# Kernel tuning notes

Hardware: AMD Instinct MI355X
Metric: run time of the kernel (lower is better)

Reference implementation:

```python
import jax, jax.numpy as jnp
import numpy as np

N_NODES = 50000
N_EDGES = 800000
HIDDEN = 64


def _init_linear(key, fan_in, fan_out):
    kw, kb = jax.random.split(key)
    lim = 1.0 / np.sqrt(fan_in)
    W = jax.random.uniform(kw, (fan_in, fan_out), jnp.float32, -lim, lim)
    b = jax.random.uniform(kb, (fan_out,), jnp.float32, -lim, lim)
    return W, b


def setup_inputs() -> dict:
    key = jax.random.key(0)
    ks = jax.random.split(key, 10)
    feat = jax.random.normal(ks[0], (N_NODES, HIDDEN), jnp.float32)
    x = jax.random.normal(ks[1], (N_NODES, 3), jnp.float32)
    src = jax.random.randint(ks[2], (N_EDGES,), 0, N_NODES, jnp.int32)
    dst = jax.random.randint(ks[3], (N_EDGES,), 0, N_NODES, jnp.int32)
    # message MLP: (2H+1) -> H -> H, relu after both layers (last_activation=mid)
    W1, b1 = _init_linear(ks[4], 2 * HIDDEN + 1, HIDDEN)
    W2, b2 = _init_linear(ks[5], HIDDEN, HIDDEN)
    # soft edge gate: H -> 1
    we, be = _init_linear(ks[6], HIDDEN, 1)
    # update MLP: H -> H -> H, relu mid, no last activation
    U1, c1 = _init_linear(ks[7], HIDDEN, HIDDEN)
    U2, c2 = _init_linear(ks[8], HIDDEN, HIDDEN)
    return dict(feat=feat, x=x, src=src, dst=dst,
                W1=W1, b1=b1, W2=W2, b2=b2, we=we, be=be,
                U1=U1, c1=c1, U2=U2, c2=c2)


def reference(feat, x, src, dst, W1, b1, W2, b2, we, be, U1, c1, U2, c2):
    # per-edge squared distance between endpoint coordinates: [E, 1]
    sqd = jnp.sum((x[src] - x[dst]) ** 2, axis=-1, keepdims=True)
    # message input: [E, 2H+1]
    msg_in = jnp.concatenate([feat[src], feat[dst], sqd], axis=-1)
    # 2-layer message MLP with relu mid and last activation
    m = jax.nn.relu(jax.nn.relu(msg_in @ W1 + b1) @ W2 + b2)
    # sigmoid soft-edge gate: [E, 1]
    gate = jax.nn.sigmoid(m @ we + be)
    # scatter-sum gated messages to destination nodes: [N, H]
    m_sum = jax.ops.segment_sum(m * gate, dst, num_segments=N_NODES)
    # node update MLP on (m_sum + feat), residual add
    h = m_sum + feat
    h_new = jax.nn.relu(h @ U1 + c1) @ U2 + c2
    return h_new + feat
```

## Files before the change

kernel.cpp:

```cpp
#include <hip/hip_runtime.h>
#include <hip/hip_bf16.h>
#include <stdint.h>

#define N_NODES 50000
#define N_EDGES 800000
#define HDIM 64
#define SCAN_N (N_NODES + 1)

#define MSUM_OFF   0
#define EP_OFF     12800000
#define DEG_OFF    (EP_OFF + 12800000)
#define OFFS_OFF   (DEG_OFF + 204800)
#define POS_OFF    (OFFS_OFF + 204800)
#define FB_OFF     (POS_OFF + 204800)
#define W1T_OFF    (FB_OFF + (size_t)N_NODES * HDIM * 2)
#define W2T_OFF    (W1T_OFF + 16384)
#define U1T_OFF    (W2T_OFF + 8192)
#define U2T_OFF    (U1T_OFF + 8192)
#define CST_OFF    (U2T_OFF + 8192)
#define WS_NEED    (CST_OFF + 4096)

#define CVT_BLOCKS   1563
#define PREPW_BLOCKS 82
#define MZ_BLOCKS    3125
#define HIST_BLOCKS  1024

typedef __attribute__((ext_vector_type(8))) short short8;
typedef __attribute__((ext_vector_type(4))) float floatx4;

__device__ __forceinline__ float bf2f(unsigned short u) {
    union { unsigned int i; float f; } v; v.i = ((unsigned int)u) << 16; return v.f;
}
__device__ __forceinline__ unsigned short f2bf(float f) {
    __hip_bfloat16 h = __float2bfloat16(f);
    return *reinterpret_cast<unsigned short*>(&h);
}

__device__ __forceinline__ int detect_is_bf16(const unsigned short* p) {
    int cnt = 0;
    #pragma unroll
    for (int i = 0; i < 64; ++i) {
        unsigned short b = p[i];
        int e = (b >> 7) & 0xFF;
        cnt += ((e >= 97 && e <= 157) || (b & 0x7FFF) == 0) ? 1 : 0;
    }
    return cnt >= 56;
}

__device__ __forceinline__ float getf(const void* p, unsigned int i, int isb) {
    return isb ? bf2f(((const unsigned short*)p)[i]) : ((const float*)p)[i];
}

__device__ __forceinline__ short8 get8bf(const void* p, unsigned int i, int isb) {
    if (isb) {
        return *reinterpret_cast<const short8*>((const short*)p + i);
    } else {
        const float4 f0 = *reinterpret_cast<const float4*>((const float*)p + i);
        const float4 f1 = *reinterpret_cast<const float4*>((const float*)p + i + 4);
        short8 a;
        a[0] = (short)f2bf(f0.x); a[1] = (short)f2bf(f0.y);
        a[2] = (short)f2bf(f0.z); a[3] = (short)f2bf(f0.w);
        a[4] = (short)f2bf(f1.x); a[5] = (short)f2bf(f1.y);
        a[6] = (short)f2bf(f1.z); a[7] = (short)f2bf(f1.w);
        return a;
    }
}

#define COMPILER_FENCE() asm volatile("" ::: "memory")
#define WAIT_LDS() __builtin_amdgcn_s_waitcnt(0xC07F)

__global__ __launch_bounds__(256) void prep_kernel(
    const void* __restrict__ feat, unsigned short* __restrict__ fb,
    const void* __restrict__ W1, const void* __restrict__ W2,
    const void* __restrict__ U1, const void* __restrict__ U2,
    const void* __restrict__ b1, const void* __restrict__ b2,
    const void* __restrict__ we, const void* __restrict__ be,
    unsigned short* __restrict__ w1t, unsigned short* __restrict__ w2t,
    unsigned short* __restrict__ u1t, unsigned short* __restrict__ u2t,
    float* __restrict__ cst,
    const int* __restrict__ dst, int* __restrict__ deg,
    uint4* __restrict__ msumz)
{
    const int b = blockIdx.x;
    if (b < CVT_BLOCKS) {
        const int isb = detect_is_bf16((const unsigned short*)feat);
        int i = (b * 256 + threadIdx.x) * 8;
        if (i >= N_NODES * HDIM) return;
        if (isb) {
            *reinterpret_cast<uint4*>(fb + i) =
                *reinterpret_cast<const uint4*>((const unsigned short*)feat + i);
        } else {
            float4 f0 = *reinterpret_cast<const float4*>((const float*)feat + i);
            float4 f1 = *reinterpret_cast<const float4*>((const float*)feat + i + 4);
            ushort4 a = {f2bf(f0.x), f2bf(f0.y), f2bf(f0.z), f2bf(f0.w)};
            ushort4 c = {f2bf(f1.x), f2bf(f1.y), f2bf(f1.z), f2bf(f1.w)};
            *reinterpret_cast<ushort4*>(fb + i)     = a;
            *reinterpret_cast<ushort4*>(fb + i + 4) = c;
        }
    } else if (b < CVT_BLOCKS + PREPW_BLOCKS) {
        const int isb = detect_is_bf16((const unsigned short*)feat);
        int idx = (b - CVT_BLOCKS) * 256 + threadIdx.x;
        if (idx < 8192) {
            int n = idx >> 7, k = idx & 127;
            w1t[idx] = f2bf(getf(W1, k * 64 + n, isb));
        } else if (idx < 12288) {
            int i = idx - 8192, n = i >> 6, k = i & 63;
            w2t[i] = f2bf(getf(W2, k * 64 + n, isb));
        } else if (idx < 16384) {
            int i = idx - 12288, n = i >> 6, k = i & 63;
            u1t[i] = f2bf(getf(U1, k * 64 + n, isb));
        } else if (idx < 20480) {
            int i = idx - 16384, n = i >> 6, k = i & 63;
            u2t[i] = f2bf(getf(U2, k * 64 + n, isb));
        } else if (idx < 20737) {
            int i = idx - 20480;
            float v;
            if (i < 64)       v = getf(b1, i, isb);
            else if (i < 128) v = getf(W1, 128 * 64 + (i - 64), isb);
            else if (i < 192) v = getf(b2, i - 128, isb);
            else if (i < 256) v = getf(we, i - 192, isb);
            else              v = getf(be, 0, isb);
            cst[i] = v;
        }
    } else if (b < CVT_BLOCKS + PREPW_BLOCKS + MZ_BLOCKS) {
        int i = (b - CVT_BLOCKS - PREPW_BLOCKS) * 256 + threadIdx.x;
        if (i < N_NODES * HDIM / 4)
            msumz[i] = (uint4){0u, 0u, 0u, 0u};
    } else {
        int e0 = (b - CVT_BLOCKS - PREPW_BLOCKS - MZ_BLOCKS) * 256 + threadIdx.x;
        for (int e = e0; e < N_EDGES; e += HIST_BLOCKS * 256)
            atomicAdd(&deg[dst[e]], 1);
    }
}

__global__ __launch_bounds__(1024) void scan_onepass_kernel(
    const int* __restrict__ deg, int* __restrict__ offs, int* __restrict__ pos)
{
    __shared__ int wsum[16];
    const int tid  = threadIdx.x;
    const int wid  = tid >> 6;
    const int lane = tid & 63;
    int run = 0;
    for (int seg = 0; seg < 49; ++seg) {
        int g = seg * 1024 + tid;
        int v = (g < SCAN_N) ? deg[g] : 0;
        int x = v;
        #pragma unroll
        for (int off = 1; off < 64; off <<= 1) {
            int t = __shfl_up(x, off);
            if (lane >= off) x += t;
        }
        if (lane == 63) wsum[wid] = x;
        __syncthreads();
        if (wid == 0) {
            int w = (lane < 16) ? wsum[lane] : 0;
            #pragma unroll
            for (int off = 1; off < 16; off <<= 1) {
                int t = __shfl_up(w, off);
                if (lane >= off) w += t;
            }
            if (lane < 16) wsum[lane] = w;
        }
        __syncthreads();
        int wexcl = (wid == 0) ? 0 : wsum[wid - 1];
        int tot   = wsum[15];
        int excl  = run + wexcl + (x - v);
        if (g < SCAN_N) { offs[g] = excl; pos[g] = excl; }
        run += tot;
        __syncthreads();
    }
}

__global__ __launch_bounds__(256) void permute_kernel(
    const void* __restrict__ feat, const void* __restrict__ xpos,
    const int* __restrict__ src, const int* __restrict__ dst,
    int* __restrict__ pos, uint4* __restrict__ epack)
{
    const int isb = detect_is_bf16((const unsigned short*)feat);
    int e = blockIdx.x * 256 + threadIdx.x;
    if (e < N_EDGES) {
        int s = src[e], d = dst[e];
        int slot = atomicAdd(&pos[d], 1);
        float dx = getf(xpos, s * 3 + 0, isb) - getf(xpos, d * 3 + 0, isb);
        float dy = getf(xpos, s * 3 + 1, isb) - getf(xpos, d * 3 + 1, isb);
        float dz = getf(xpos, s * 3 + 2, isb) - getf(xpos, d * 3 + 2, isb);
        float sqd = dx * dx + dy * dy + dz * dz;
        uint4 p;
        p.x = (unsigned int)s;
        p.y = (unsigned int)d;
        p.z = __float_as_uint(sqd);
        p.w = 0u;
        epack[slot] = p;
    }
}

template <bool CSR>
__global__ __launch_bounds__(512, 4) void edge_kernel(
    const unsigned short* __restrict__ fbf,
    const unsigned short* __restrict__ w1t, const unsigned short* __restrict__ w2t,
    const float* __restrict__ cst,
    const void* __restrict__ feat, const void* __restrict__ xpos,
    const int* __restrict__ src, const int* __restrict__ dst,
    const uint4* __restrict__ epack,
    const void* __restrict__ W1, const void* __restrict__ b1,
    const void* __restrict__ W2, const void* __restrict__ b2,
    const void* __restrict__ we, const void* __restrict__ be,
    float* __restrict__ msum, unsigned int msum_cap)
{
    __shared__ __align__(16) short sW1[16][64][8];
    __shared__ __align__(16) short sW2[8][64][8];
    __shared__ __align__(16) short sA2[2][8][16][72];

    const int tid  = threadIdx.x;
    const int wave = tid >> 6;
    const int lane = tid & 63;
    const int l15  = lane & 15;
    const int quad = lane >> 4;
    const int rowb = quad * 4;

    float b1r[4], w1lr[4], b2r[4], wer[4];
    float ber;
    short8 bw1[4][4];
    short8 bw2[2][4];

    if constexpr (CSR) {
        for (int i = tid; i < 16 * 64; i += 512) {
            int f = i >> 6, l = i & 63;
            int n = (f & 3) * 16 + (l & 15);
            int k0 = (f >> 2) * 32 + (l >> 4) * 8;
            *reinterpret_cast<short8*>(&sW1[f][l][0]) =
                *reinterpret_cast<const short8*>(w1t + n * 128 + k0);
        }
        for (int i = tid; i < 8 * 64; i += 512) {
            int f = i >> 6, l = i & 63;
            int n = (f & 3) * 16 + (l & 15);
            int k0 = (f >> 2) * 32 + (l >> 4) * 8;
            *reinterpret_cast<short8*>(&sW2[f][l][0]) =
                *reinterpret_cast<const short8*>(w2t + n * 64 + k0);
        }
        #pragma unroll
        for (int nt = 0; nt < 4; ++nt) {
            int n = nt * 16 + l15;
            b1r[nt]  = cst[n];
            w1lr[nt] = cst[64 + n];
            b2r[nt]  = cst[128 + n];
            wer[nt]  = cst[192 + n];
        }
        ber = cst[256];
        __syncthreads();

        const int nbiter = N_EDGES / 256;
        for (int it = blockIdx.x; it < nbiter; it += gridDim.x) {
            const int ebase = it * 256 + wave * 16;

            int sidx = 0, didx = 0;
            float sqd = 0.f;
            if (lane < 32) {
                int e = ebase + l15 + ((lane >> 4) << 7);
                uint4 p = epack[e];
                sidx = (int)p.x;
                didx = (int)p.y;
                sqd  = __uint_as_float(p.z);
            }
            const int snA = __shfl(sidx, l15);
            const int dnA = __shfl(didx, l15);
            const int snB = __shfl(sidx, l15 + 16);
            const int dnB = __shfl(didx, l15 + 16);

            short8 caA[4], caB[4];
            #pragma unroll
            for (int c = 0; c < 4; ++c) {
                const int nA = (c < 2) ? snA : dnA;
                const int nB = (c < 2) ? snB : dnB;
                caA[c] = *reinterpret_cast<const short8*>(
                    (const short*)fbf + (unsigned int)nA * 64u + (c & 1) * 32 + quad * 8);
                caB[c] = *reinterpret_cast<const short8*>(
                    (const short*)fbf + (unsigned int)nB * 64u + (c & 1) * 32 + quad * 8);
            }

            floatx4 accA[4], accB[4];
            #pragma unroll
            for (int nt = 0; nt < 4; ++nt) {
                accA[nt] = (floatx4){0.f, 0.f, 0.f, 0.f};
                accB[nt] = (floatx4){0.f, 0.f, 0.f, 0.f};
            }
            #pragma unroll
            for (int c = 0; c < 4; ++c) {
                #pragma unroll
                for (int nt = 0; nt < 4; ++nt) {
                    short8 wb = *reinterpret_cast<const short8*>(&sW1[c * 4 + nt][lane][0]);
                    accA[nt] = __builtin_amdgcn_mfma_f32_16x16x32_bf16(caA[c], wb, accA[nt], 0, 0, 0);
                    accB[nt] = __builtin_amdgcn_mfma_f32_16x16x32_bf16(caB[c], wb, accB[nt], 0, 0, 0);
                }
            }

            float sqA[4], sqB[4];
            #pragma unroll
            for (int r = 0; r < 4; ++r) {
                sqA[r] = __shfl(sqd, rowb + r);
                sqB[r] = __shfl(sqd, 16 + rowb + r);
            }
            #pragma unroll
            for (int nt = 0; nt < 4; ++nt)
                #pragma unroll
                for (int r = 0; r < 4; ++r) {
                    float vA = fmaxf(accA[nt][r] + b1r[nt] + sqA[r] * w1lr[nt], 0.f);
                    float vB = fmaxf(accB[nt][r] + b1r[nt] + sqB[r] * w1lr[nt], 0.f);
                    sA2[0][wave][rowb + r][nt * 16 + l15] = (short)f2bf(vA);
                    sA2[1][wave][rowb + r][nt * 16 + l15] = (short)f2bf(vB);
                }
            COMPILER_FENCE();
            WAIT_LDS();

            floatx4 acc2A[4], acc2B[4];
            #pragma unroll
            for (int nt = 0; nt < 4; ++nt) {
                acc2A[nt] = (floatx4){0.f, 0.f, 0.f, 0.f};
                acc2B[nt] = (floatx4){0.f, 0.f, 0.f, 0.f};
            }
            #pragma unroll
            for (int c = 0; c < 2; ++c) {
                short8 aA = *reinterpret_cast<const short8*>(&sA2[0][wave][l15][c * 32 + quad * 8]);
                short8 aB = *reinterpret_cast<const short8*>(&sA2[1][wave][l15][c * 32 + quad * 8]);
                #pragma unroll
                for (int nt = 0; nt < 4; ++nt) {
                    short8 wb = *reinterpret_cast<const short8*>(&sW2[c * 4 + nt][lane][0]);
                    acc2A[nt] = __builtin_amdgcn_mfma_f32_16x16x32_bf16(aA, wb, acc2A[nt], 0, 0, 0);
                    acc2B[nt] = __builtin_amdgcn_mfma_f32_16x16x32_bf16(aB, wb, acc2B[nt], 0, 0, 0);
                }
            }
            COMPILER_FENCE();

            float mvA[4][4], mvB[4][4];
            float pA[4] = {0.f, 0.f, 0.f, 0.f};
            float pB[4] = {0.f, 0.f, 0.f, 0.f};
            #pragma unroll
            for (int nt = 0; nt < 4; ++nt)
                #pragma unroll
                for (int r = 0; r < 4; ++r) {
                    float vA = fmaxf(acc2A[nt][r] + b2r[nt], 0.f);
                    float vB = fmaxf(acc2B[nt][r] + b2r[nt], 0.f);
                    mvA[nt][r] = vA;
                    mvB[nt][r] = vB;
                    pA[r] += vA * wer[nt];
                    pB[r] += vB * wer[nt];
                }
            #pragma unroll
            for (int off = 1; off < 16; off <<= 1)
                #pragma unroll
                for (int r = 0; r < 4; ++r) {
                    pA[r] += __shfl_xor(pA[r], off);
                    pB[r] += __shfl_xor(pB[r], off);
                }
            float gA[4], gB[4];
            #pragma unroll
            for (int r = 0; r < 4; ++r) {
                gA[r] = 1.f / (1.f + __expf(-(pA[r] + ber)));
                gB[r] = 1.f / (1.f + __expf(-(pB[r] + ber)));
            }

            int grp = (lane >> 4) & 1;
            int nd = __shfl(didx, grp * 16 + ((l15 + 1) & 15));
            int flag = (lane < 32) && ((l15 == 15) || (nd != didx));
            unsigned long long bal = __ballot(flag);
            unsigned int mA = (unsigned int)(bal & 0xFFFFull);
            unsigned int mB = (unsigned int)((bal >> 16) & 0xFFFFull);

            int lo = 0;
            while (mA) {
                int hi = __ffs(mA) - 1;
                float s0 = 0.f, s1 = 0.f, s2 = 0.f, s3 = 0.f;
                #pragma unroll
                for (int r = 0; r < 4; ++r) {
                    int gr = rowb + r;
                    float g = (gr >= lo && gr <= hi) ? gA[r] : 0.f;
                    s0 += g * mvA[0][r];
                    s1 += g * mvA[1][r];
                    s2 += g * mvA[2][r];
                    s3 += g * mvA[3][r];
                }
                s0 += __shfl_xor(s0, 16); s0 += __shfl_xor(s0, 32);
                s1 += __shfl_xor(s1, 16); s1 += __shfl_xor(s1, 32);
                s2 += __shfl_xor(s2, 16); s2 += __shfl_xor(s2, 32);
                s3 += __shfl_xor(s3, 16); s3 += __shfl_xor(s3, 32);
                int d = __shfl(didx, hi);
                float v = (quad == 0) ? s0 : (quad == 1) ? s1 : (quad == 2) ? s2 : s3;
                unsafeAtomicAdd(&msum[(unsigned int)d * 64u + (unsigned int)quad * 16u + l15], v);
                lo = hi + 1;
                mA &= mA - 1;
            }
            lo = 0;
            while (mB) {
                int hi = __ffs(mB) - 1;
                float s0 = 0.f, s1 = 0.f, s2 = 0.f, s3 = 0.f;
                #pragma unroll
                for (int r = 0; r < 4; ++r) {
                    int gr = rowb + r;
                    float g = (gr >= lo && gr <= hi) ? gB[r] : 0.f;
                    s0 += g * mvB[0][r];
                    s1 += g * mvB[1][r];
                    s2 += g * mvB[2][r];
                    s3 += g * mvB[3][r];
                }
                s0 += __shfl_xor(s0, 16); s0 += __shfl_xor(s0, 32);
                s1 += __shfl_xor(s1, 16); s1 += __shfl_xor(s1, 32);
                s2 += __shfl_xor(s2, 16); s2 += __shfl_xor(s2, 32);
                s3 += __shfl_xor(s3, 16); s3 += __shfl_xor(s3, 32);
                int d = __shfl(didx, 16 + hi);
                float v = (quad == 0) ? s0 : (quad == 1) ? s1 : (quad == 2) ? s2 : s3;
                unsafeAtomicAdd(&msum[(unsigned int)d * 64u + (unsigned int)quad * 16u + l15], v);
                lo = hi + 1;
                mB &= mB - 1;
            }
        }
    } else {
        const int isb = detect_is_bf16((const unsigned short*)feat);
        #pragma unroll
        for (int c = 0; c < 4; ++c)
            #pragma unroll
            for (int nt = 0; nt < 4; ++nt) {
                short8 b;
                #pragma unroll
                for (int j = 0; j < 8; ++j)
                    b[j] = (short)f2bf(getf(W1, (c * 32 + quad * 8 + j) * 64 + nt * 16 + l15, isb));
                bw1[c][nt] = b;
            }
        #pragma unroll
        for (int c = 0; c < 2; ++c)
            #pragma unroll
            for (int nt = 0; nt < 4; ++nt) {
                short8 b;
                #pragma unroll
                for (int j = 0; j < 8; ++j)
                    b[j] = (short)f2bf(getf(W2, (c * 32 + quad * 8 + j) * 64 + nt * 16 + l15, isb));
                bw2[c][nt] = b;
            }
        #pragma unroll
        for (int nt = 0; nt < 4; ++nt) {
            int n = nt * 16 + l15;
            b1r[nt]  = getf(b1, n, isb);
            w1lr[nt] = getf(W1, 128 * 64 + n, isb);
            b2r[nt]  = getf(b2, n, isb);
            wer[nt]  = getf(we, n, isb);
        }
        ber = getf(be, 0, isb);

        const int ntiles = N_EDGES / 128;
        for (int t = blockIdx.x; t < ntiles; t += gridDim.x) {
            const int ebase = t * 128 + wave * 16;
            int sidx = 0, didx = 0;
            float sqd = 0.f;
            if (lane < 16) {
                int e = ebase + lane;
                sidx = src[e];
                didx = dst[e];
                float dx = getf(xpos, sidx * 3 + 0, isb) - getf(xpos, didx * 3 + 0, isb);
                float dy = getf(xpos, sidx * 3 + 1, isb) - getf(xpos, didx * 3 + 1, isb);
                float dz = getf(xpos, sidx * 3 + 2, isb) - getf(xpos, didx * 3 + 2, isb);
                sqd = dx * dx + dy * dy + dz * dz;
            }
            const int sn     = __shfl(sidx, l15);
            const int dn_row = __shfl(didx, l15);

            floatx4 acc[4];
            #pragma unroll
            for (int nt = 0; nt < 4; ++nt) acc[nt] = (floatx4){0.f, 0.f, 0.f, 0.f};
            #pragma unroll
            for (int c = 0; c < 4; ++c) {
                const int node = (c < 2) ? sn : dn_row;
                const unsigned int aoff = (unsigned int)node * 64u + (c & 1) * 32 + quad * 8;
                short8 a = get8bf(feat, aoff, isb);
                #pragma unroll
                for (int nt = 0; nt < 4; ++nt)
                    acc[nt] = __builtin_amdgcn_mfma_f32_16x16x32_bf16(a, bw1[c][nt], acc[nt], 0, 0, 0);
            }

            float sq[4];
            #pragma unroll
            for (int r = 0; r < 4; ++r) sq[r] = __shfl(sqd, rowb + r);
            #pragma unroll
            for (int nt = 0; nt < 4; ++nt)
                #pragma unroll
                for (int r = 0; r < 4; ++r) {
                    float v = fmaxf(acc[nt][r] + b1r[nt] + sq[r] * w1lr[nt], 0.f);
                    sA2[0][wave][rowb + r][nt * 16 + l15] = (short)f2bf(v);
                }
            COMPILER_FENCE();
            WAIT_LDS();

            floatx4 acc2[4];
            #pragma unroll
            for (int nt = 0; nt < 4; ++nt) acc2[nt] = (floatx4){0.f, 0.f, 0.f, 0.f};
            #pragma unroll
            for (int c = 0; c < 2; ++c) {
                short8 a = *reinterpret_cast<const short8*>(&sA2[0][wave][l15][c * 32 + quad * 8]);
                #pragma unroll
                for (int nt = 0; nt < 4; ++nt)
                    acc2[nt] = __builtin_amdgcn_mfma_f32_16x16x32_bf16(a, bw2[c][nt], acc2[nt], 0, 0, 0);
            }
            COMPILER_FENCE();

            float mval[4][4];
            float part[4] = {0.f, 0.f, 0.f, 0.f};
            #pragma unroll
            for (int nt = 0; nt < 4; ++nt)
                #pragma unroll
                for (int r = 0; r < 4; ++r) {
                    float v = fmaxf(acc2[nt][r] + b2r[nt], 0.f);
                    mval[nt][r] = v;
                    part[r] += v * wer[nt];
                }
            #pragma unroll
            for (int off = 1; off < 16; off <<= 1)
                #pragma unroll
                for (int r = 0; r < 4; ++r) part[r] += __shfl_xor(part[r], off);
            float gate[4];
            #pragma unroll
            for (int r = 0; r < 4; ++r)
                gate[r] = 1.f / (1.f + __expf(-(part[r] + ber)));

            #pragma unroll
            for (int r = 0; r < 4; ++r) {
                int dn = __shfl(didx, rowb + r);
                unsigned int base = (unsigned int)dn * 64u;
                if (base + 64u <= msum_cap) {
                    #pragma unroll
                    for (int nt = 0; nt < 4; ++nt)
                        unsafeAtomicAdd(&msum[base + nt * 16 + l15], mval[nt][r] * gate[r]);
                }
            }
        }
    }
}

__global__ __launch_bounds__(256, 2) void node_kernel(
    const float* __restrict__ msum,
    const unsigned short* __restrict__ u1t, const unsigned short* __restrict__ u2t,
    const void* __restrict__ feat,
    const void* __restrict__ U1, const void* __restrict__ c1v,
    const void* __restrict__ U2, const void* __restrict__ c2v,
    void* __restrict__ out)
{
    __shared__ __align__(16) short sT[4][16][72];
    __shared__ __align__(16) float sF[4][16][68];

    const int isb  = detect_is_bf16((const unsigned short*)feat);
    const int tid  = threadIdx.x;
    const int wave = tid >> 6;
    const int lane = tid & 63;
    const int l15  = lane & 15;
    const int quad = lane >> 4;

    short8 u1f[2][4], u2f[2][4];
    if (u1t) {
        #pragma unroll
        for (int nt = 0; nt < 4; ++nt) {
            const int n = nt * 16 + l15;
            #pragma unroll
            for (int c = 0; c < 2; ++c) {
                u1f[c][nt] = *reinterpret_cast<const short8*>(u1t + n * 64 + c * 32 + quad * 8);
                u2f[c][nt] = *reinterpret_cast<const short8*>(u2t + n * 64 + c * 32 + quad * 8);
            }
        }
    } else {
        #pragma unroll
        for (int c = 0; c < 2; ++c)
            #pragma unroll
            for (int nt = 0; nt < 4; ++nt) {
                short8 a, b;
                #pragma unroll
                for (int j = 0; j < 8; ++j) {
                    int k = c * 32 + quad * 8 + j, n = nt * 16 + l15;
                    a[j] = (short)f2bf(getf(U1, k * 64 + n, isb));
                    b[j] = (short)f2bf(getf(U2, k * 64 + n, isb));
                }
                u1f[c][nt] = a; u2f[c][nt] = b;
            }
    }
    float c1r[4], c2r[4];
    #pragma unroll
    for (int nt = 0; nt < 4; ++nt) {
        c1r[nt] = getf(c1v, nt * 16 + l15, isb);
        c2r[nt] = getf(c2v, nt * 16 + l15, isb);
    }
    const int rowb = quad * 4;

    const int ntile = (N_NODES + 15) / 16;
    const int t = blockIdx.x * 4 + wave;
    if (t < ntile) {
        const int node = t * 16 + l15;

        short8 ah[2];
        #pragma unroll
        for (int c = 0; c < 2; ++c) {
            unsigned int off = (unsigned int)node * 64u + c * 32 + quad * 8;
            float4 m0 = *reinterpret_cast<const float4*>(msum + off);
            float4 m1 = *reinterpret_cast<const float4*>(msum + off + 4);
            float mv[8] = {m0.x, m0.y, m0.z, m0.w, m1.x, m1.y, m1.z, m1.w};
            float hv[8];
            if (isb) {
                short8 fv = *reinterpret_cast<const short8*>((const short*)feat + off);
                #pragma unroll
                for (int j = 0; j < 8; ++j) hv[j] = bf2f((unsigned short)fv[j]);
            } else {
                float4 f0 = *reinterpret_cast<const float4*>((const float*)feat + off);
                float4 f1 = *reinterpret_cast<const float4*>((const float*)feat + off + 4);
                hv[0] = f0.x; hv[1] = f0.y; hv[2] = f0.z; hv[3] = f0.w;
                hv[4] = f1.x; hv[5] = f1.y; hv[6] = f1.z; hv[7] = f1.w;
            }
            short8 a;
            #pragma unroll
            for (int j = 0; j < 8; ++j) a[j] = (short)f2bf(mv[j] + hv[j]);
            ah[c] = a;
        }

        floatx4 acc[4];
        #pragma unroll
        for (int nt = 0; nt < 4; ++nt) acc[nt] = (floatx4){0.f, 0.f, 0.f, 0.f};
        #pragma unroll
        for (int c = 0; c < 2; ++c)
            #pragma unroll
            for (int nt = 0; nt < 4; ++nt)
                acc[nt] = __builtin_amdgcn_mfma_f32_16x16x32_bf16(ah[c], u1f[c][nt], acc[nt], 0, 0, 0);

        #pragma unroll
        for (int nt = 0; nt < 4; ++nt)
            #pragma unroll
            for (int r = 0; r < 4; ++r) {
                float v = fmaxf(acc[nt][r] + c1r[nt], 0.f);
                sT[wave][rowb + r][nt * 16 + l15] = (short)f2bf(v);
            }
        COMPILER_FENCE();
        WAIT_LDS();

        floatx4 acc2[4];
        #pragma unroll
        for (int nt = 0; nt < 4; ++nt) acc2[nt] = (floatx4){0.f, 0.f, 0.f, 0.f};
        #pragma unroll
        for (int c = 0; c < 2; ++c) {
            short8 a = *reinterpret_cast<const short8*>(&sT[wave][l15][c * 32 + quad * 8]);
            #pragma unroll
            for (int nt = 0; nt < 4; ++nt)
                acc2[nt] = __builtin_amdgcn_mfma_f32_16x16x32_bf16(a, u2f[c][nt], acc2[nt], 0, 0, 0);
        }
        COMPILER_FENCE();

        #pragma unroll
        for (int nt = 0; nt < 4; ++nt)
            #pragma unroll
            for (int r = 0; r < 4; ++r)
                sF[wave][rowb + r][nt * 16 + l15] = acc2[nt][r] + c2r[nt];
        COMPILER_FENCE();
        WAIT_LDS();

        const unsigned int ob = (unsigned int)node * 64u + quad * 16;
        if (isb) {
            const unsigned short* fp = (const unsigned short*)feat + ob;
            unsigned short* op = (unsigned short*)out + ob;
            #pragma unroll
            for (int k = 0; k < 2; ++k) {
                ushort4 o0, o1;
                float4 v0 = *reinterpret_cast<const float4*>(&sF[wave][l15][quad * 16 + k * 8]);
                float4 v1 = *reinterpret_cast<const float4*>(&sF[wave][l15][quad * 16 + k * 8 + 4]);
                const ushort4 f0 = *reinterpret_cast<const ushort4*>(fp + k * 8);
                const ushort4 f1 = *reinterpret_cast<const ushort4*>(fp + k * 8 + 4);
                o0.x = f2bf(v0.x + bf2f(f0.x)); o0.y = f2bf(v0.y + bf2f(f0.y));
                o0.z = f2bf(v0.z + bf2f(f0.z)); o0.w = f2bf(v0.w + bf2f(f0.w));
                o1.x = f2bf(v1.x + bf2f(f1.x)); o1.y = f2bf(v1.y + bf2f(f1.y));
                o1.z = f2bf(v1.z + bf2f(f1.z)); o1.w = f2bf(v1.w + bf2f(f1.w));
                *reinterpret_cast<ushort4*>(op + k * 8)     = o0;
                *reinterpret_cast<ushort4*>(op + k * 8 + 4) = o1;
            }
        } else {
            const float* fp = (const float*)feat + ob;
            float* op = (float*)out + ob;
            #pragma unroll
            for (int k = 0; k < 4; ++k) {
                float4 v = *reinterpret_cast<const float4*>(&sF[wave][l15][quad * 16 + k * 4]);
                float4 f = *reinterpret_cast<const float4*>(fp + k * 4);
                float4 o = {v.x + f.x, v.y + f.y, v.z + f.z, v.w + f.w};
                *reinterpret_cast<float4*>(op + k * 4) = o;
            }
        }
        COMPILER_FENCE();
    }
}

extern "C" void kernel_launch(void* const* d_in, const int* in_sizes, int n_in,
                              void* d_out, int out_size, void* d_ws, size_t ws_size,
                              hipStream_t stream) {
    const void* feat = d_in[0];
    const void* x    = d_in[1];
    const int* src   = (const int*)d_in[2];
    const int* dst   = (const int*)d_in[3];
    const void* W1   = d_in[4];
    const void* b1   = d_in[5];
    const void* W2   = d_in[6];
    const void* b2   = d_in[7];
    const void* we   = d_in[8];
    const void* be   = d_in[9];
    const void* U1   = d_in[10];
    const void* c1   = d_in[11];
    const void* U2   = d_in[12];
    const void* c2   = d_in[13];
    char* ws = (char*)d_ws;

    if (ws_size >= WS_NEED) {
        float* msum = (float*)(ws + MSUM_OFF);
        uint4* epack = (uint4*)(ws + EP_OFF);
        int* deg  = (int*)(ws + DEG_OFF);
        int* offs = (int*)(ws + OFFS_OFF);
        int* pos  = (int*)(ws + POS_OFF);
        unsigned short* fb  = (unsigned short*)(ws + FB_OFF);
        unsigned short* w1t = (unsigned short*)(ws + W1T_OFF);
        unsigned short* w2t = (unsigned short*)(ws + W2T_OFF);
        unsigned short* u1t = (unsigned short*)(ws + U1T_OFF);
        unsigned short* u2t = (unsigned short*)(ws + U2T_OFF);
        float* cst = (float*)(ws + CST_OFF);

        hipMemsetAsync(deg, 0, 204800, stream);
        prep_kernel<<<CVT_BLOCKS + PREPW_BLOCKS + MZ_BLOCKS + HIST_BLOCKS, 256, 0, stream>>>(
            feat, fb, W1, W2, U1, U2, b1, b2, we, be,
            w1t, w2t, u1t, u2t, cst, dst, deg, (uint4*)msum);
        scan_onepass_kernel<<<1, 1024, 0, stream>>>(deg, offs, pos);
        permute_kernel<<<(N_EDGES + 255) / 256, 256, 0, stream>>>(feat, x, src, dst, pos, epack);
        edge_kernel<true><<<625, 512, 0, stream>>>(fb, w1t, w2t, cst, feat, x, src, dst, epack,
                                                   W1, b1, W2, b2, we, be,
                                                   msum, (unsigned int)(N_NODES * HDIM));
        node_kernel<<<((N_NODES + 15) / 16 + 3) / 4, 256, 0, stream>>>(
            msum, u1t, u2t, feat, U1, c1, U2, c2, d_out);
    } else {
        float* msum = (float*)ws;
        size_t need = (size_t)N_NODES * HDIM * sizeof(float);
        size_t clr  = need < ws_size ? need : ws_size;
        unsigned int cap = (unsigned int)(ws_size / sizeof(float));
        if (cap > (unsigned int)(N_NODES * HDIM)) cap = (unsigned int)(N_NODES * HDIM);

        hipMemsetAsync(msum, 0, clr, stream);
        edge_kernel<false><<<1250, 512, 0, stream>>>(nullptr, nullptr, nullptr, nullptr,
                                                     feat, x, src, dst,
                                                     nullptr, W1, b1, W2, b2, we, be,
                                                     msum, cap);
        node_kernel<<<((N_NODES + 15) / 16 + 3) / 4, 256, 0, stream>>>(
            msum, nullptr, nullptr, feat, U1, c1, U2, c2, d_out);
    }
}
```

Measured before the change: 296.0 us.

## Split scan into three kernels, halve LDS staging, raise edge kernel occupancy

Replaces the single-block serial scan with a three-kernel block-sum, serial-partials and local-scan scheme. In the edge kernel it processes the A and B halves sequentially through one shared LDS staging buffer, raises the launch-bounds waves-per-EU hint from 4 to 6 and increases the grid from 625 to 768 blocks. It also switches float-to-bf16 conversions to an inline v_cvt_pk_bf16_f32 instruction and rewrites the accumulations as explicit fmaf. The goal is more occupancy and less serial scan latency, at the cost of extra launches, more LDS syncs between the halves and possible register pressure under the tighter bound.

Result: faster. 276.4 us (-6.6%).

```diff
diff --git a/kernel.cpp b/kernel.cpp
--- a/kernel.cpp
+++ b/kernel.cpp
@@ -34,6 +34,11 @@
 __device__ __forceinline__ unsigned short f2bf(float f) {
     __hip_bfloat16 h = __float2bfloat16(f);
     return *reinterpret_cast<unsigned short*>(&h);
+}
+__device__ __forceinline__ unsigned short f2bf_fast(float f) {
+    unsigned int r;
+    asm("v_cvt_pk_bf16_f32 %0, %1, %1" : "=v"(r) : "v"(f));
+    return (unsigned short)r;
 }
 
 __device__ __forceinline__ int detect_is_bf16(const unsigned short* p) {
@@ -133,42 +138,40 @@
     }
 }
 
-__global__ __launch_bounds__(1024) void scan_onepass_kernel(
-    const int* __restrict__ deg, int* __restrict__ offs, int* __restrict__ pos)
-{
-    __shared__ int wsum[16];
-    const int tid  = threadIdx.x;
-    const int wid  = tid >> 6;
-    const int lane = tid & 63;
-    int run = 0;
-    for (int seg = 0; seg < 49; ++seg) {
-        int g = seg * 1024 + tid;
-        int v = (g < SCAN_N) ? deg[g] : 0;
-        int x = v;
-        #pragma unroll
-        for (int off = 1; off < 64; off <<= 1) {
-            int t = __shfl_up(x, off);
-            if (lane >= off) x += t;
-        }
-        if (lane == 63) wsum[wid] = x;
+__global__ void scan1_kernel(const int* __restrict__ deg, int* __restrict__ part) {
+    __shared__ int s[1024];
+    int g = blockIdx.x * 1024 + threadIdx.x;
+    s[threadIdx.x] = (g < SCAN_N) ? deg[g] : 0;
+    __syncthreads();
+    for (int off = 512; off > 0; off >>= 1) {
+        if (threadIdx.x < off) s[threadIdx.x] += s[threadIdx.x + off];
         __syncthreads();
-        if (wid == 0) {
-            int w = (lane < 16) ? wsum[lane] : 0;
-            #pragma unroll
-            for (int off = 1; off < 16; off <<= 1) {
-                int t = __shfl_up(w, off);
-                if (lane >= off) w += t;
-            }
-            if (lane < 16) wsum[lane] = w;
-        }
+    }
+    if (threadIdx.x == 0) part[blockIdx.x] = s[0];
+}
+
+__global__ void scan2_kernel(int* __restrict__ part, int nparts) {
+    if (threadIdx.x == 0) {
+        int run = 0;
+        for (int i = 0; i < nparts; ++i) { int t = part[i]; part[i] = run; run += t; }
+    }
+}
+
+__global__ void scan3_kernel(const int* __restrict__ deg, const int* __restrict__ part,
+                             int* __restrict__ offs, int* __restrict__ pos) {
+    __shared__ int s[1024];
+    int g = blockIdx.x * 1024 + threadIdx.x;
+    int v = (g < SCAN_N) ? deg[g] : 0;
+    s[threadIdx.x] = v;
+    __syncthreads();
+    for (int off = 1; off < 1024; off <<= 1) {
+        int t = (threadIdx.x >= off) ? s[threadIdx.x - off] : 0;
         __syncthreads();
-        int wexcl = (wid == 0) ? 0 : wsum[wid - 1];
-        int tot   = wsum[15];
-        int excl  = run + wexcl + (x - v);
-        if (g < SCAN_N) { offs[g] = excl; pos[g] = excl; }
-        run += tot;
+        s[threadIdx.x] += t;
         __syncthreads();
     }
+    int excl = s[threadIdx.x] - v + part[blockIdx.x];
+    if (g < SCAN_N) { offs[g] = excl; pos[g] = excl; }
 }
 
 __global__ __launch_bounds__(256) void permute_kernel(
@@ -195,7 +198,7 @@
 }
 
 template <bool CSR>
-__global__ __launch_bounds__(512, 4) void edge_kernel(
+__global__ __launch_bounds__(512, 6) void edge_kernel(
     const unsigned short* __restrict__ fbf,
     const unsigned short* __restrict__ w1t, const unsigned short* __restrict__ w2t,
     const float* __restrict__ cst,
@@ -209,7 +212,7 @@
 {
     __shared__ __align__(16) short sW1[16][64][8];
     __shared__ __align__(16) short sW2[8][64][8];
-    __shared__ __align__(16) short sA2[2][8][16][72];
+    __shared__ __align__(16) short sA2[8][16][72];
 
     const int tid  = threadIdx.x;
     const int wave = tid >> 6;
@@ -300,32 +303,51 @@
                 sqA[r] = __shfl(sqd, rowb + r);
                 sqB[r] = __shfl(sqd, 16 + rowb + r);
             }
+
             #pragma unroll
             for (int nt = 0; nt < 4; ++nt)
                 #pragma unroll
                 for (int r = 0; r < 4; ++r) {
-                    float vA = fmaxf(accA[nt][r] + b1r[nt] + sqA[r] * w1lr[nt], 0.f);
-                    float vB = fmaxf(accB[nt][r] + b1r[nt] + sqB[r] * w1lr[nt], 0.f);
-                    sA2[0][wave][rowb + r][nt * 16 + l15] = (short)f2bf(vA);
-                    sA2[1][wave][rowb + r][nt * 16 + l15] = (short)f2bf(vB);
+                    float vA = fmaxf(fmaf(sqA[r], w1lr[nt], accA[nt][r]) + b1r[nt], 0.f);
+                    sA2[wave][rowb + r][nt * 16 + l15] = (short)f2bf_fast(vA);
                 }
             COMPILER_FENCE();
             WAIT_LDS();
 
-            floatx4 acc2A[4], acc2B[4];
-            #pragma unroll
-            for (int nt = 0; nt < 4; ++nt) {
-                acc2A[nt] = (floatx4){0.f, 0.f, 0.f, 0.f};
-                acc2B[nt] = (floatx4){0.f, 0.f, 0.f, 0.f};
-            }
+            floatx4 acc2A[4];
+            #pragma unroll
+            for (int nt = 0; nt < 4; ++nt) acc2A[nt] = (floatx4){0.f, 0.f, 0.f, 0.f};
             #pragma unroll
             for (int c = 0; c < 2; ++c) {
-                short8 aA = *reinterpret_cast<const short8*>(&sA2[0][wave][l15][c * 32 + quad * 8]);
-                short8 aB = *reinterpret_cast<const short8*>(&sA2[1][wave][l15][c * 32 + quad * 8]);
+                short8 aA = *reinterpret_cast<const short8*>(&sA2[wave][l15][c * 32 + quad * 8]);
                 #pragma unroll
                 for (int nt = 0; nt < 4; ++nt) {
                     short8 wb = *reinterpret_cast<const short8*>(&sW2[c * 4 + nt][lane][0]);
                     acc2A[nt] = __builtin_amdgcn_mfma_f32_16x16x32_bf16(aA, wb, acc2A[nt], 0, 0, 0);
+                }
+            }
+            COMPILER_FENCE();
+            WAIT_LDS();
+
+            #pragma unroll
+            for (int nt = 0; nt < 4; ++nt)
+                #pragma unroll
+                for (int r = 0; r < 4; ++r) {
+                    float vB = fmaxf(fmaf(sqB[r], w1lr[nt], accB[nt][r]) + b1r[nt], 0.f);
+                    sA2[wave][rowb + r][nt * 16 + l15] = (short)f2bf_fast(vB);
+                }
+            COMPILER_FENCE();
+            WAIT_LDS();
+
+            floatx4 acc2B[4];
+            #pragma unroll
+            for (int nt = 0; nt < 4; ++nt) acc2B[nt] = (floatx4){0.f, 0.f, 0.f, 0.f};
+            #pragma unroll
+            for (int c = 0; c < 2; ++c) {
+                short8 aB = *reinterpret_cast<const short8*>(&sA2[wave][l15][c * 32 + quad * 8]);
+                #pragma unroll
+                for (int nt = 0; nt < 4; ++nt) {
+                    short8 wb = *reinterpret_cast<const short8*>(&sW2[c * 4 + nt][lane][0]);
                     acc2B[nt] = __builtin_amdgcn_mfma_f32_16x16x32_bf16(aB, wb, acc2B[nt], 0, 0, 0);
                 }
             }
@@ -342,8 +364,8 @@
                     float vB = fmaxf(acc2B[nt][r] + b2r[nt], 0.f);
                     mvA[nt][r] = vA;
                     mvB[nt][r] = vB;
-                    pA[r] += vA * wer[nt];
-                    pB[r] += vB * wer[nt];
+                    pA[r] = fmaf(vA, wer[nt], pA[r]);
+                    pB[r] = fmaf(vB, wer[nt], pB[r]);
                 }
             #pragma unroll
             for (int off = 1; off < 16; off <<= 1)
@@ -374,10 +396,10 @@
                 for (int r = 0; r < 4; ++r) {
                     int gr = rowb + r;
                     float g = (gr >= lo && gr <= hi) ? gA[r] : 0.f;
-                    s0 += g * mvA[0][r];
-                    s1 += g * mvA[1][r];
-                    s2 += g * mvA[2][r];
-                    s3 += g * mvA[3][r];
+                    s0 = fmaf(g, mvA[0][r], s0);
+                    s1 = fmaf(g, mvA[1][r], s1);
+                    s2 = fmaf(g, mvA[2][r], s2);
+                    s3 = fmaf(g, mvA[3][r], s3);
                 }
                 s0 += __shfl_xor(s0, 16); s0 += __shfl_xor(s0, 32);
                 s1 += __shfl_xor(s1, 16); s1 += __shfl_xor(s1, 32);
@@ -397,10 +419,10 @@
                 for (int r = 0; r < 4; ++r) {
                     int gr = rowb + r;
                     float g = (gr >= lo && gr <= hi) ? gB[r] : 0.f;
-                    s0 += g * mvB[0][r];
-                    s1 += g * mvB[1][r];
-                    s2 += g * mvB[2][r];
-                    s3 += g * mvB[3][r];
+                    s0 = fmaf(g, mvB[0][r], s0);
+                    s1 = fmaf(g, mvB[1][r], s1);
+                    s2 = fmaf(g, mvB[2][r], s2);
+                    s3 = fmaf(g, mvB[3][r], s3);
                 }
                 s0 += __shfl_xor(s0, 16); s0 += __shfl_xor(s0, 32);
                 s1 += __shfl_xor(s1, 16); s1 += __shfl_xor(s1, 32);
@@ -483,7 +505,7 @@
                 #pragma unroll
                 for (int r = 0; r < 4; ++r) {
                     float v = fmaxf(acc[nt][r] + b1r[nt] + sq[r] * w1lr[nt], 0.f);
-                    sA2[0][wave][rowb + r][nt * 16 + l15] = (short)f2bf(v);
+                    sA2[wave][rowb + r][nt * 16 + l15] = (short)f2bf(v);
                 }
             COMPILER_FENCE();
             WAIT_LDS();
@@ -493,12 +515,13 @@
             for (int nt = 0; nt < 4; ++nt) acc2[nt] = (floatx4){0.f, 0.f, 0.f, 0.f};
             #pragma unroll
             for (int c = 0; c < 2; ++c) {
-                short8 a = *reinterpret_cast<const short8*>(&sA2[0][wave][l15][c * 32 + quad * 8]);
+                short8 a = *reinterpret_cast<const short8*>(&sA2[wave][l15][c * 32 + quad * 8]);
                 #pragma unroll
                 for (int nt = 0; nt < 4; ++nt)
                     acc2[nt] = __builtin_amdgcn_mfma_f32_16x16x32_bf16(a, bw2[c][nt], acc2[nt], 0, 0, 0);
             }
             COMPILER_FENCE();
+            WAIT_LDS();
 
             float mval[4][4];
             float part[4] = {0.f, 0.f, 0.f, 0.f};
@@ -610,7 +633,7 @@
             }
             short8 a;
             #pragma unroll
-            for (int j = 0; j < 8; ++j) a[j] = (short)f2bf(mv[j] + hv[j]);
+            for (int j = 0; j < 8; ++j) a[j] = (short)f2bf_fast(mv[j] + hv[j]);
             ah[c] = a;
         }
 
@@ -628,7 +651,7 @@
             #pragma unroll
             for (int r = 0; r < 4; ++r) {
                 float v = fmaxf(acc[nt][r] + c1r[nt], 0.f);
-                sT[wave][rowb + r][nt * 16 + l15] = (short)f2bf(v);
+                sT[wave][rowb + r][nt * 16 + l15] = (short)f2bf_fast(v);
             }
         COMPILER_FENCE();
         WAIT_LDS();
@@ -664,10 +687,10 @@
                 float4 v1 = *reinterpret_cast<const float4*>(&sF[wave][l15][quad * 16 + k * 8 + 4]);
                 const ushort4 f0 = *reinterpret_cast<const ushort4*>(fp + k * 8);
                 const ushort4 f1 = *reinterpret_cast<const ushort4*>(fp + k * 8 + 4);
-                o0.x = f2bf(v0.x + bf2f(f0.x)); o0.y = f2bf(v0.y + bf2f(f0.y));
-                o0.z = f2bf(v0.z + bf2f(f0.z)); o0.w = f2bf(v0.w + bf2f(f0.w));
-                o1.x = f2bf(v1.x + bf2f(f1.x)); o1.y = f2bf(v1.y + bf2f(f1.y));
-                o1.z = f2bf(v1.z + bf2f(f1.z)); o1.w = f2bf(v1.w + bf2f(f1.w));
+                o0.x = f2bf_fast(v0.x + bf2f(f0.x)); o0.y = f2bf_fast(v0.y + bf2f(f0.y));
+                o0.z = f2bf_fast(v0.z + bf2f(f0.z)); o0.w = f2bf_fast(v0.w + bf2f(f0.w));
+                o1.x = f2bf_fast(v1.x + bf2f(f1.x)); o1.y = f2bf_fast(v1.y + bf2f(f1.y));
+                o1.z = f2bf_fast(v1.z + bf2f(f1.z)); o1.w = f2bf_fast(v1.w + bf2f(f1.w));
                 *reinterpret_cast<ushort4*>(op + k * 8)     = o0;
                 *reinterpret_cast<ushort4*>(op + k * 8 + 4) = o1;
             }
@@ -722,9 +745,11 @@
         prep_kernel<<<CVT_BLOCKS + PREPW_BLOCKS + MZ_BLOCKS + HIST_BLOCKS, 256, 0, stream>>>(
             feat, fb, W1, W2, U1, U2, b1, b2, we, be,
             w1t, w2t, u1t, u2t, cst, dst, deg, (uint4*)msum);
-        scan_onepass_kernel<<<1, 1024, 0, stream>>>(deg, offs, pos);
+        scan1_kernel<<<49, 1024, 0, stream>>>(deg, offs + 51200 - 64);
+        scan2_kernel<<<1, 64, 0, stream>>>(offs + 51200 - 64, 49);
+        scan3_kernel<<<49, 1024, 0, stream>>>(deg, offs + 51200 - 64, offs, pos);
         permute_kernel<<<(N_EDGES + 255) / 256, 256, 0, stream>>>(feat, x, src, dst, pos, epack);
-        edge_kernel<true><<<625, 512, 0, stream>>>(fb, w1t, w2t, cst, feat, x, src, dst, epack,
+        edge_kernel<true><<<768, 512, 0, stream>>>(fb, w1t, w2t, cst, feat, x, src, dst, epack,
                                                    W1, b1, W2, b2, we, be,
                                                    msum, (unsigned int)(N_NODES * HDIM));
         node_kernel<<<((N_NODES + 15) / 16 + 3) / 4, 256, 0, stream>>>(
```
